# Kernel tuning notes

Measured on AMD Instinct MI355X. Metric: run time of the kernel, lower is better.

## Reference

```python
import jax, jax.numpy as jnp
import numpy as np

RBF_DIM = 64          # args.radius_emb_dim
FOLD_DIM = 128        # args.fold_dim
PROT_RADIUS = 30.0    # args.protein_radius (GaussianSmearing stop)
NP_, NL_, E_ = 100000, 50000, 500000


def gaussian_smearing(d):
    # GaussianSmearing(start=0, stop=PROT_RADIUS, num_gaussians=RBF_DIM)
    offsets = jnp.linspace(0.0, PROT_RADIUS, RBF_DIM, dtype=d.dtype)  # [R]
    coeff = -0.5 / (offsets[1] - offsets[0]) ** 2
    return jnp.exp(coeff * (d[:, None] - offsets[None, :]) ** 2)  # [E, R]


def setup_inputs() -> dict:
    key = jax.random.key(0)
    ks = jax.random.split(key, 12)
    scale = 10.0  # spread positions so distances span [0, PROT_RADIUS]
    pos = lambda k, n: jax.random.normal(k, (n, 3), jnp.float32) * scale
    inp = {
        'lig_pos': pos(ks[0], NL_),
        'prot_pos': pos(ks[1], NP_),
        'prot_pos_Cb': pos(ks[2], NP_),
        'prot_pos_C': pos(ks[3], NP_),
        'prot_pos_O': pos(ks[4], NP_),
        'prot_pos_N': pos(ks[5], NP_),
        'W1': jax.random.normal(ks[6], (5 * RBF_DIM, FOLD_DIM), jnp.float32) * 0.05,
        'b1': jnp.zeros((FOLD_DIM,), jnp.float32),
        'W2': jax.random.normal(ks[7], (FOLD_DIM, FOLD_DIM), jnp.float32) * 0.05,
        'b2': jnp.zeros((FOLD_DIM,), jnp.float32),
        'src': jax.random.randint(ks[8], (E_,), 0, NL_, jnp.int32),   # ligand index per edge
        'dst': jax.random.randint(ks[9], (E_,), 0, NP_, jnp.int32),   # protein index per edge
    }
    return inp


def reference(lig_pos, prot_pos, prot_pos_Cb, prot_pos_C, prot_pos_O, prot_pos_N,
              W1, b1, W2, b2, src, dst):
    lp = lig_pos[src]  # [E, 3] gather of ligand positions
    # 5 distance channels: CA/Cb/C/O/N protein atoms, each RBF-smeared
    feats = [gaussian_smearing(jnp.linalg.norm(lp - p[dst], axis=-1))
             for p in (prot_pos, prot_pos_Cb, prot_pos_C, prot_pos_O, prot_pos_N)]
    edge_attr = jnp.concatenate(feats, axis=-1)  # [E, 5*RBF_DIM]
    h = jax.nn.relu(edge_attr @ W1 + b1)         # [E, FOLD_DIM]
    return h @ W2 + b2                           # [E, FOLD_DIM]
```

## Files before the change

### kernel.cpp

```cpp
#include <hip/hip_runtime.h>
#include <hip/hip_bf16.h>

typedef unsigned short ushort_t;
typedef unsigned int uint_t;
typedef __attribute__((ext_vector_type(8))) short short8;
typedef __attribute__((ext_vector_type(4))) float f32x4;
typedef __attribute__((ext_vector_type(4))) uint_t uint4_t;
typedef __attribute__((ext_vector_type(2))) uint_t uint2_t;

#define FOLD 128
#define S_CONST 1.78357580f
#define DS_CONST 0.84932180f

__device__ __forceinline__ ushort_t f2bf(float f) {
    uint_t x = __builtin_bit_cast(uint_t, f);
    x += 0x7FFFu + ((x >> 16) & 1u);
    return (ushort_t)(x >> 16);
}

__device__ __forceinline__ uint_t pkbf(float a, float b) {
    uint_t xl = __builtin_bit_cast(uint_t, a);
    uint_t xh = __builtin_bit_cast(uint_t, b);
    uint_t rl = (xl + 0x7FFFu + ((xl >> 16) & 1u)) >> 16;
    uint_t rh = (xh + 0x7FFFu + ((xh >> 16) & 1u)) & 0xFFFF0000u;
    return rh | rl;
}

__global__ __launch_bounds__(256) void pack_w(const float* __restrict__ W1,
                                              const float* __restrict__ W2,
                                              ushort_t* __restrict__ W1p,
                                              ushort_t* __restrict__ W2p) {
    int i = blockIdx.x * 256 + threadIdx.x;
    if (i < 40960) {
        int j = i & 7, l = (i >> 3) & 63, nt = (i >> 9) & 7, ks = i >> 12;
        int row = ks * 32 + ((l >> 4) << 3) + j;
        int col = nt * 16 + (l & 15);
        W1p[i] = f2bf(W1[row * FOLD + col]);
    } else if (i < 40960 + 16384) {
        int q = i - 40960;
        int j = q & 7, l = (q >> 3) & 63, nt = (q >> 9) & 7, ks = q >> 12;
        int row = ks * 32 + ((l >> 4) << 3) + j;
        int col = nt * 16 + (l & 15);
        W2p[q] = f2bf(W2[row * FOLD + col]);
    }
}

__global__ __launch_bounds__(256, 2) void fused(
    const float* __restrict__ lig,
    const float* __restrict__ p0, const float* __restrict__ p1,
    const float* __restrict__ p2, const float* __restrict__ p3,
    const float* __restrict__ p4,
    const ushort_t* __restrict__ W1p, const ushort_t* __restrict__ W2p,
    const float* __restrict__ b1, const float* __restrict__ b2,
    const int* __restrict__ src, const int* __restrict__ dst,
    float* __restrict__ out, int E)
{
    __shared__ float d_lds[2][5][32];
    __shared__ alignas(16) uint_t attrU[32 * 160];
    __shared__ alignas(16) uint_t h_u[32 * 64];

    const int t = threadIdx.x;
    const int w = t >> 6;
    const int l = t & 63;
    const int lrow = l & 15, lgrp = l >> 4;
    const int aswz = (lrow & 7) << 2;
    const int ntiles = (E + 31) >> 5;

    const short8* W1v = reinterpret_cast<const short8*>(W1p);
    const short8* W2v = reinterpret_cast<const short8*>(W2p);
    short8 wb1[20], wb2[8];
    #pragma unroll
    for (int ks = 0; ks < 10; ++ks) {
        wb1[2 * ks]     = W1v[(ks * 8 + w * 2 + 0) * 64 + l];
        wb1[2 * ks + 1] = W1v[(ks * 8 + w * 2 + 1) * 64 + l];
    }
    #pragma unroll
    for (int ks = 0; ks < 4; ++ks) {
        wb2[2 * ks]     = W2v[(ks * 8 + w * 2 + 0) * 64 + l];
        wb2[2 * ks + 1] = W2v[(ks * 8 + w * 2 + 1) * 64 + l];
    }
    f32x4 hb1[2], hb2[2];
    hb1[0] = *reinterpret_cast<const f32x4*>(&b1[w * 32 + lgrp * 4]);
    hb1[1] = *reinterpret_cast<const f32x4*>(&b1[w * 32 + 16 + lgrp * 4]);
    hb2[0] = *reinterpret_cast<const f32x4*>(&b2[w * 32 + lgrp * 4]);
    hb2[1] = *reinterpret_cast<const f32x4*>(&b2[w * 32 + 16 + lgrp * 4]);

    const bool gth = (t < 160);
    const int gm = t & 31, gc = t >> 5;
    const float* P = (gc == 0) ? p0 : (gc == 1) ? p1 : (gc == 2) ? p2 : (gc == 3) ? p3 : p4;

    const int m2 = t >> 3, q2 = t & 7;
    const int swz = (m2 & 7) << 2;
    const float ubase = (float)(8 * q2) * DS_CONST;

    int tile = blockIdx.x;
    if (tile >= ntiles) return;

    if (gth) {
        int e = tile * 32 + gm; if (e >= E) e = E - 1;
        int s = src[e], dd = dst[e];
        float dx = lig[3 * s]     - P[3 * dd];
        float dy = lig[3 * s + 1] - P[3 * dd + 1];
        float dz = lig[3 * s + 2] - P[3 * dd + 2];
        d_lds[0][gc][gm] = sqrtf(dx * dx + dy * dy + dz * dz);
    }
    __syncthreads();

    int buf = 0;
    while (true) {
        const int next = tile + gridDim.x;
        const bool havenext = (next < ntiles);

        float ax, ay, az, bx, by, bz;
        if (gth && havenext) {
            int e = next * 32 + gm; if (e >= E) e = E - 1;
            int s = src[e], dd = dst[e];
            ax = lig[3 * s];     bx = P[3 * dd];
            ay = lig[3 * s + 1]; by = P[3 * dd + 1];
            az = lig[3 * s + 2]; bz = P[3 * dd + 2];
        }

        float dv[5];
        #pragma unroll
        for (int c = 0; c < 5; ++c) dv[c] = d_lds[buf][c][m2];
        #pragma unroll
        for (int c = 0; c < 5; ++c) {
            float u0 = __builtin_fmaf(dv[c], S_CONST, -ubase);
            uint4_t vals;
            #pragma unroll
            for (int i = 0; i < 4; ++i) {
                float ua = u0 - (float)(2 * i) * DS_CONST;
                float ub = u0 - (float)(2 * i + 1) * DS_CONST;
                float va = __builtin_amdgcn_exp2f(-(ua * ua));
                float vb = __builtin_amdgcn_exp2f(-(ub * ub));
                vals[i] = pkbf(va, vb);
            }
            int o = 32 * c + 4 * q2;
            *reinterpret_cast<uint4_t*>(&attrU[m2 * 160 + (o ^ swz)]) = vals;
        }

        if (gth && havenext) {
            float dx = ax - bx, dy = ay - by, dz = az - bz;
            d_lds[buf ^ 1][gc][gm] = sqrtf(dx * dx + dy * dy + dz * dz);
        }
        __syncthreads();

        f32x4 g1[2][2] = {{{0.f,0.f,0.f,0.f},{0.f,0.f,0.f,0.f}},
                          {{0.f,0.f,0.f,0.f},{0.f,0.f,0.f,0.f}}};
        #pragma unroll
        for (int ks = 0; ks < 10; ++ks) {
            int o = ks * 16 + lgrp * 4;
            short8 af0 = *reinterpret_cast<const short8*>(&attrU[lrow * 160 + (o ^ aswz)]);
            short8 af1 = *reinterpret_cast<const short8*>(&attrU[(lrow + 16) * 160 + (o ^ aswz)]);
            g1[0][0] = __builtin_amdgcn_mfma_f32_16x16x32_bf16(wb1[2 * ks],     af0, g1[0][0], 0, 0, 0);
            g1[0][1] = __builtin_amdgcn_mfma_f32_16x16x32_bf16(wb1[2 * ks],     af1, g1[0][1], 0, 0, 0);
            g1[1][0] = __builtin_amdgcn_mfma_f32_16x16x32_bf16(wb1[2 * ks + 1], af0, g1[1][0], 0, 0, 0);
            g1[1][1] = __builtin_amdgcn_mfma_f32_16x16x32_bf16(wb1[2 * ks + 1], af1, g1[1][1], 0, 0, 0);
        }

        #pragma unroll
        for (int nh = 0; nh < 2; ++nh) {
            #pragma unroll
            for (int eh = 0; eh < 2; ++eh) {
                float v0 = fmaxf(g1[nh][eh][0] + hb1[nh][0], 0.f);
                float v1 = fmaxf(g1[nh][eh][1] + hb1[nh][1], 0.f);
                float v2 = fmaxf(g1[nh][eh][2] + hb1[nh][2], 0.f);
                float v3 = fmaxf(g1[nh][eh][3] + hb1[nh][3], 0.f);
                uint2_t pv;
                pv[0] = pkbf(v0, v1);
                pv[1] = pkbf(v2, v3);
                int e = eh * 16 + lrow;
                int dw = (w * 16 + nh * 8 + lgrp * 2) ^ ((e & 7) << 2);
                *reinterpret_cast<uint2_t*>(&h_u[e * 64 + dw]) = pv;
            }
        }
        __syncthreads();

        f32x4 o2[2][2] = {{{0.f,0.f,0.f,0.f},{0.f,0.f,0.f,0.f}},
                          {{0.f,0.f,0.f,0.f},{0.f,0.f,0.f,0.f}}};
        #pragma unroll
        for (int ks = 0; ks < 4; ++ks) {
            int dw = ks * 16 + lgrp * 4;
            short8 hf0 = *reinterpret_cast<const short8*>(&h_u[lrow * 64 + (dw ^ aswz)]);
            short8 hf1 = *reinterpret_cast<const short8*>(&h_u[(lrow + 16) * 64 + (dw ^ aswz)]);
            o2[0][0] = __builtin_amdgcn_mfma_f32_16x16x32_bf16(wb2[2 * ks],     hf0, o2[0][0], 0, 0, 0);
            o2[0][1] = __builtin_amdgcn_mfma_f32_16x16x32_bf16(wb2[2 * ks],     hf1, o2[0][1], 0, 0, 0);
            o2[1][0] = __builtin_amdgcn_mfma_f32_16x16x32_bf16(wb2[2 * ks + 1], hf0, o2[1][0], 0, 0, 0);
            o2[1][1] = __builtin_amdgcn_mfma_f32_16x16x32_bf16(wb2[2 * ks + 1], hf1, o2[1][1], 0, 0, 0);
        }

        const int e0i = tile * 32;
        #pragma unroll
        for (int nh = 0; nh < 2; ++nh) {
            #pragma unroll
            for (int eh = 0; eh < 2; ++eh) {
                int e = e0i + eh * 16 + lrow;
                if (e < E) {
                    f32x4 v = o2[nh][eh] + hb2[nh];
                    *reinterpret_cast<f32x4*>(&out[(size_t)e * FOLD + w * 32 + nh * 16 + lgrp * 4]) = v;
                }
            }
        }

        if (!havenext) break;
        tile = next;
        buf ^= 1;
    }
}

extern "C" void kernel_launch(void* const* d_in, const int* in_sizes, int n_in,
                              void* d_out, int out_size, void* d_ws, size_t ws_size,
                              hipStream_t stream) {
    const float* lig = (const float*)d_in[0];
    const float* p0  = (const float*)d_in[1];
    const float* p1  = (const float*)d_in[2];
    const float* p2  = (const float*)d_in[3];
    const float* p3  = (const float*)d_in[4];
    const float* p4  = (const float*)d_in[5];
    const float* W1  = (const float*)d_in[6];
    const float* b1  = (const float*)d_in[7];
    const float* W2  = (const float*)d_in[8];
    const float* b2  = (const float*)d_in[9];
    const int* src   = (const int*)d_in[10];
    const int* dst   = (const int*)d_in[11];
    float* out = (float*)d_out;
    const int E = in_sizes[10];

    ushort_t* W1p = (ushort_t*)d_ws;
    ushort_t* W2p = W1p + 40960;

    pack_w<<<(40960 + 16384 + 255) / 256, 256, 0, stream>>>(W1, W2, W1p, W2p);

    int tiles = (E + 31) / 32;
    int nblk = tiles < 512 ? tiles : 512;
    fused<<<nblk, 256, 0, stream>>>(lig, p0, p1, p2, p3, p4, W1p, W2p,
                                    b1, b2, src, dst, out, E);
}
```

Measured before the change: 129.5 us.

## Double edge tile to 64 per block and rebalance gather threads

Each block iteration now processes 64 edges instead of 32, so the register-resident weight fragments are reused across twice as many MFMA tiles and barriers are amortized over more work. The distance gather is reorganized so all 256 threads compute four channels and the first 64 also compute the fifth, replacing the 160-thread scheme. Grid cap rises to 1024 blocks. LDS use and accumulator registers double, which may hurt occupancy under the 2-blocks-per-SIMD launch bound.

```diff
diff --git a/kernel.cpp b/kernel.cpp
--- a/kernel.cpp
+++ b/kernel.cpp
@@ -45,6 +45,8 @@
     }
 }
 
+#define TEDGE 64
+
 __global__ __launch_bounds__(256, 2) void fused(
     const float* __restrict__ lig,
     const float* __restrict__ p0, const float* __restrict__ p1,
@@ -55,16 +57,16 @@
     const int* __restrict__ src, const int* __restrict__ dst,
     float* __restrict__ out, int E)
 {
-    __shared__ float d_lds[2][5][32];
-    __shared__ alignas(16) uint_t attrU[32 * 160];
-    __shared__ alignas(16) uint_t h_u[32 * 64];
+    __shared__ float d_lds[2][5][TEDGE];
+    __shared__ alignas(16) uint_t attrU[TEDGE * 160];
+    __shared__ alignas(16) uint_t h_u[TEDGE * 64];
 
     const int t = threadIdx.x;
     const int w = t >> 6;
     const int l = t & 63;
     const int lrow = l & 15, lgrp = l >> 4;
     const int aswz = (lrow & 7) << 2;
-    const int ntiles = (E + 31) >> 5;
+    const int ntiles = (E + TEDGE - 1) / TEDGE;
 
     const short8* W1v = reinterpret_cast<const short8*>(W1p);
     const short8* W2v = reinterpret_cast<const short8*>(W2p);
@@ -85,24 +87,30 @@
     hb2[0] = *reinterpret_cast<const f32x4*>(&b2[w * 32 + lgrp * 4]);
     hb2[1] = *reinterpret_cast<const f32x4*>(&b2[w * 32 + 16 + lgrp * 4]);
 
-    const bool gth = (t < 160);
-    const int gm = t & 31, gc = t >> 5;
-    const float* P = (gc == 0) ? p0 : (gc == 1) ? p1 : (gc == 2) ? p2 : (gc == 3) ? p3 : p4;
+    const int g1c = t >> 6, g1m = t & 63;
+    const bool gth2 = (t < 64);
+    const float* GP1 = (g1c == 0) ? p0 : (g1c == 1) ? p1 : (g1c == 2) ? p2 : p3;
+    const float* GP2 = p4;
 
     const int m2 = t >> 3, q2 = t & 7;
-    const int swz = (m2 & 7) << 2;
     const float ubase = (float)(8 * q2) * DS_CONST;
 
     int tile = blockIdx.x;
     if (tile >= ntiles) return;
 
-    if (gth) {
-        int e = tile * 32 + gm; if (e >= E) e = E - 1;
+    {
+        int e = tile * TEDGE + g1m; if (e >= E) e = E - 1;
         int s = src[e], dd = dst[e];
-        float dx = lig[3 * s]     - P[3 * dd];
-        float dy = lig[3 * s + 1] - P[3 * dd + 1];
-        float dz = lig[3 * s + 2] - P[3 * dd + 2];
-        d_lds[0][gc][gm] = sqrtf(dx * dx + dy * dy + dz * dz);
+        float dx = lig[3 * s]     - GP1[3 * dd];
+        float dy = lig[3 * s + 1] - GP1[3 * dd + 1];
+        float dz = lig[3 * s + 2] - GP1[3 * dd + 2];
+        d_lds[0][g1c][g1m] = sqrtf(dx * dx + dy * dy + dz * dz);
+        if (gth2) {
+            float ex = lig[3 * s]     - GP2[3 * dd];
+            float ey = lig[3 * s + 1] - GP2[3 * dd + 1];
+            float ez = lig[3 * s + 2] - GP2[3 * dd + 2];
+            d_lds[0][4][g1m] = sqrtf(ex * ex + ey * ey + ez * ez);
+        }
     }
     __syncthreads();
 
@@ -111,57 +119,75 @@
         const int next = tile + gridDim.x;
         const bool havenext = (next < ntiles);
 
-        float ax, ay, az, bx, by, bz;
-        if (gth && havenext) {
-            int e = next * 32 + gm; if (e >= E) e = E - 1;
+        float ax, ay, az, bx, by, bz, cx, cy, cz;
+        if (havenext) {
+            int e = next * TEDGE + g1m; if (e >= E) e = E - 1;
             int s = src[e], dd = dst[e];
-            ax = lig[3 * s];     bx = P[3 * dd];
-            ay = lig[3 * s + 1]; by = P[3 * dd + 1];
-            az = lig[3 * s + 2]; bz = P[3 * dd + 2];
-        }
-
-        float dv[5];
-        #pragma unroll
-        for (int c = 0; c < 5; ++c) dv[c] = d_lds[buf][c][m2];
-        #pragma unroll
-        for (int c = 0; c < 5; ++c) {
-            float u0 = __builtin_fmaf(dv[c], S_CONST, -ubase);
-            uint4_t vals;
-            #pragma unroll
-            for (int i = 0; i < 4; ++i) {
-                float ua = u0 - (float)(2 * i) * DS_CONST;
-                float ub = u0 - (float)(2 * i + 1) * DS_CONST;
-                float va = __builtin_amdgcn_exp2f(-(ua * ua));
-                float vb = __builtin_amdgcn_exp2f(-(ub * ub));
-                vals[i] = pkbf(va, vb);
-            }
-            int o = 32 * c + 4 * q2;
-            *reinterpret_cast<uint4_t*>(&attrU[m2 * 160 + (o ^ swz)]) = vals;
-        }
-
-        if (gth && havenext) {
+            ax = lig[3 * s];     bx = GP1[3 * dd];
+            ay = lig[3 * s + 1]; by = GP1[3 * dd + 1];
+            az = lig[3 * s + 2]; bz = GP1[3 * dd + 2];
+            if (gth2) {
+                cx = GP2[3 * dd]; cy = GP2[3 * dd + 1]; cz = GP2[3 * dd + 2];
+            }
+        }
+
+        #pragma unroll
+        for (int half = 0; half < 2; ++half) {
+            const int m = m2 + half * 32;
+            const int swz = (m & 7) << 2;
+            float dv[5];
+            #pragma unroll
+            for (int c = 0; c < 5; ++c) dv[c] = d_lds[buf][c][m];
+            #pragma unroll
+            for (int c = 0; c < 5; ++c) {
+                float u0 = __builtin_fmaf(dv[c], S_CONST, -ubase);
+                uint4_t vals;
+                #pragma unroll
+                for (int i = 0; i < 4; ++i) {
+                    float ua = u0 - (float)(2 * i) * DS_CONST;
+                    float ub = u0 - (float)(2 * i + 1) * DS_CONST;
+                    float va = __builtin_amdgcn_exp2f(-(ua * ua));
+                    float vb = __builtin_amdgcn_exp2f(-(ub * ub));
+                    vals[i] = pkbf(va, vb);
+                }
+                int o = 32 * c + 4 * q2;
+                *reinterpret_cast<uint4_t*>(&attrU[m * 160 + (o ^ swz)]) = vals;
+            }
+        }
+
+        if (havenext) {
             float dx = ax - bx, dy = ay - by, dz = az - bz;
-            d_lds[buf ^ 1][gc][gm] = sqrtf(dx * dx + dy * dy + dz * dz);
+            d_lds[buf ^ 1][g1c][g1m] = sqrtf(dx * dx + dy * dy + dz * dz);
+            if (gth2) {
+                float ex = ax - cx, ey = ay - cy, ez = az - cz;
+                d_lds[buf ^ 1][4][g1m] = sqrtf(ex * ex + ey * ey + ez * ez);
+            }
         }
         __syncthreads();
 
-        f32x4 g1[2][2] = {{{0.f,0.f,0.f,0.f},{0.f,0.f,0.f,0.f}},
-                          {{0.f,0.f,0.f,0.f},{0.f,0.f,0.f,0.f}}};
+        f32x4 g1[2][4];
+        #pragma unroll
+        for (int nh = 0; nh < 2; ++nh)
+            #pragma unroll
+            for (int eh = 0; eh < 4; ++eh) g1[nh][eh] = f32x4{0.f, 0.f, 0.f, 0.f};
         #pragma unroll
         for (int ks = 0; ks < 10; ++ks) {
             int o = ks * 16 + lgrp * 4;
-            short8 af0 = *reinterpret_cast<const short8*>(&attrU[lrow * 160 + (o ^ aswz)]);
-            short8 af1 = *reinterpret_cast<const short8*>(&attrU[(lrow + 16) * 160 + (o ^ aswz)]);
-            g1[0][0] = __builtin_amdgcn_mfma_f32_16x16x32_bf16(wb1[2 * ks],     af0, g1[0][0], 0, 0, 0);
-            g1[0][1] = __builtin_amdgcn_mfma_f32_16x16x32_bf16(wb1[2 * ks],     af1, g1[0][1], 0, 0, 0);
-            g1[1][0] = __builtin_amdgcn_mfma_f32_16x16x32_bf16(wb1[2 * ks + 1], af0, g1[1][0], 0, 0, 0);
-            g1[1][1] = __builtin_amdgcn_mfma_f32_16x16x32_bf16(wb1[2 * ks + 1], af1, g1[1][1], 0, 0, 0);
+            short8 af[4];
+            #pragma unroll
+            for (int eh = 0; eh < 4; ++eh)
+                af[eh] = *reinterpret_cast<const short8*>(&attrU[(lrow + eh * 16) * 160 + (o ^ aswz)]);
+            #pragma unroll
+            for (int eh = 0; eh < 4; ++eh) {
+                g1[0][eh] = __builtin_amdgcn_mfma_f32_16x16x32_bf16(wb1[2 * ks],     af[eh], g1[0][eh], 0, 0, 0);
+                g1[1][eh] = __builtin_amdgcn_mfma_f32_16x16x32_bf16(wb1[2 * ks + 1], af[eh], g1[1][eh], 0, 0, 0);
+            }
         }
 
         #pragma unroll
         for (int nh = 0; nh < 2; ++nh) {
             #pragma unroll
-            for (int eh = 0; eh < 2; ++eh) {
+            for (int eh = 0; eh < 4; ++eh) {
                 float v0 = fmaxf(g1[nh][eh][0] + hb1[nh][0], 0.f);
                 float v1 = fmaxf(g1[nh][eh][1] + hb1[nh][1], 0.f);
                 float v2 = fmaxf(g1[nh][eh][2] + hb1[nh][2], 0.f);
@@ -176,24 +202,30 @@
         }
         __syncthreads();
 
-        f32x4 o2[2][2] = {{{0.f,0.f,0.f,0.f},{0.f,0.f,0.f,0.f}},
-                          {{0.f,0.f,0.f,0.f},{0.f,0.f,0.f,0.f}}};
+        f32x4 o2[2][4];
+        #pragma unroll
+        for (int nh = 0; nh < 2; ++nh)
+            #pragma unroll
+            for (int eh = 0; eh < 4; ++eh) o2[nh][eh] = f32x4{0.f, 0.f, 0.f, 0.f};
         #pragma unroll
         for (int ks = 0; ks < 4; ++ks) {
             int dw = ks * 16 + lgrp * 4;
-            short8 hf0 = *reinterpret_cast<const short8*>(&h_u[lrow * 64 + (dw ^ aswz)]);
-            short8 hf1 = *reinterpret_cast<const short8*>(&h_u[(lrow + 16) * 64 + (dw ^ aswz)]);
-            o2[0][0] = __builtin_amdgcn_mfma_f32_16x16x32_bf16(wb2[2 * ks],     hf0, o2[0][0], 0, 0, 0);
-            o2[0][1] = __builtin_amdgcn_mfma_f32_16x16x32_bf16(wb2[2 * ks],     hf1, o2[0][1], 0, 0, 0);
-            o2[1][0] = __builtin_amdgcn_mfma_f32_16x16x32_bf16(wb2[2 * ks + 1], hf0, o2[1][0], 0, 0, 0);
-            o2[1][1] = __builtin_amdgcn_mfma_f32_16x16x32_bf16(wb2[2 * ks + 1], hf1, o2[1][1], 0, 0, 0);
-        }
-
-        const int e0i = tile * 32;
+            short8 hf[4];
+            #pragma unroll
+            for (int eh = 0; eh < 4; ++eh)
+                hf[eh] = *reinterpret_cast<const short8*>(&h_u[(lrow + eh * 16) * 64 + (dw ^ aswz)]);
+            #pragma unroll
+            for (int eh = 0; eh < 4; ++eh) {
+                o2[0][eh] = __builtin_amdgcn_mfma_f32_16x16x32_bf16(wb2[2 * ks],     hf[eh], o2[0][eh], 0, 0, 0);
+                o2[1][eh] = __builtin_amdgcn_mfma_f32_16x16x32_bf16(wb2[2 * ks + 1], hf[eh], o2[1][eh], 0, 0, 0);
+            }
+        }
+
+        const int e0i = tile * TEDGE;
         #pragma unroll
         for (int nh = 0; nh < 2; ++nh) {
             #pragma unroll
-            for (int eh = 0; eh < 2; ++eh) {
+            for (int eh = 0; eh < 4; ++eh) {
                 int e = e0i + eh * 16 + lrow;
                 if (e < E) {
                     f32x4 v = o2[nh][eh] + hb2[nh];
@@ -231,8 +263,8 @@
 
     pack_w<<<(40960 + 16384 + 255) / 256, 256, 0, stream>>>(W1, W2, W1p, W2p);
 
-    int tiles = (E + 31) / 32;
-    int nblk = tiles < 512 ? tiles : 512;
+    int tiles = (E + TEDGE - 1) / TEDGE;
+    int nblk = tiles < 1024 ? tiles : 1024;
     fused<<<nblk, 256, 0, stream>>>(lig, p0, p1, p2, p3, p4, W1p, W2p,
                                     b1, b2, src, dst, out, E);
 }
```

After: 126.9 us. 2.1% less time.
